# Optimization experiments

Hardware: AMD Instinct MI355X
Metric: run time of the kernel (lower is better)

The kernel has to match this reference:

```python
import jax, jax.numpy as jnp
import numpy as np

B, S, F, D, I, NH, L, K = 8, 512, 64, 512, 1024, 8, 2, 4
DH = I // NH  # 128
H1, OUT = 32, 24


def setup_inputs() -> dict:
    key = jax.random.key(0)
    ks = iter(jax.random.split(key, 48))
    def nrm(shape, s=0.02):
        return jax.random.normal(next(ks), shape, jnp.float32) * s
    return {
        "x": jax.random.normal(next(ks), (B, S, F), jnp.float32),
        "in_w": nrm((F, D)), "in_b": jnp.zeros((D,), jnp.float32),
        "ln_w": jnp.ones((L, D), jnp.float32), "ln_b": jnp.zeros((L, D), jnp.float32),
        "up_w": nrm((L, D, 2 * I)),
        "conv_w": nrm((L, I, K), 0.1), "conv_b": jnp.zeros((L, I), jnp.float32),
        "q_w": nrm((L, I, I)), "k_w": nrm((L, I, I)), "v_w": nrm((L, I, I)),
        "ig_w": nrm((L, 3 * I, NH)), "ig_b": nrm((L, NH), 0.1),
        "fg_w": nrm((L, 3 * I, NH)),
        "fg_b": jnp.tile(jnp.linspace(3.0, 6.0, NH, dtype=jnp.float32)[None], (L, 1)),
        "gn_w": jnp.ones((L, I), jnp.float32),
        "skip_w": jnp.ones((L, I), jnp.float32),
        "down_w": nrm((L, I, D)),
        "post_w": jnp.ones((D,), jnp.float32), "post_b": jnp.zeros((D,), jnp.float32),
        "h1_w": nrm((D, H1)), "h1_b": jnp.zeros((H1,), jnp.float32),
        "h2_w": nrm((H1, OUT)), "h2_b": jnp.zeros((OUT,), jnp.float32),
    }


def _layernorm(x, w, b, eps=1e-5):
    mu = x.mean(-1, keepdims=True)
    var = x.var(-1, keepdims=True)
    return (x - mu) * jax.lax.rsqrt(var + eps) * w + b


def _mlstm(q, k, v, ig, fg):
    # q,k,v: (B,NH,S,DH); ig,fg: (B,NH,S). Parallel exponential-gated matrix memory.
    logf = jax.nn.log_sigmoid(fg)
    cs = jnp.cumsum(logf, axis=-1)                      # (B,NH,S)
    dmat = cs[..., :, None] - cs[..., None, :]          # sum_{j=s+1..t} log f_j
    mask = jnp.tril(jnp.ones((S, S), bool))
    log_fg_mat = jnp.where(mask, dmat, -jnp.inf)
    log_D = log_fg_mat + ig[..., None, :]               # add i-gate at source pos
    max_d = jnp.max(log_D, axis=-1, keepdims=True)      # (B,NH,S,1) stabilizer m
    Dm = jnp.exp(log_D - max_d)
    qk = jnp.einsum('bnsd,bntd->bnst', q, k) / jnp.sqrt(jnp.float32(DH))
    Cmat = qk * Dm
    norm = jnp.maximum(jnp.abs(Cmat.sum(-1, keepdims=True)), jnp.exp(-max_d))
    return jnp.einsum('bnst,bntd->bnsd', Cmat / (norm + 1e-6), v)


def _forward(x, in_w, in_b, ln_w, ln_b, up_w, conv_w, conv_b, q_w, k_w, v_w,
             ig_w, ig_b, fg_w, fg_b, gn_w, skip_w, down_w, post_w, post_b,
             h1_w, h1_b, h2_w, h2_b):
    h = x @ in_w + in_b                                  # input_proj: (B,S,D)
    for l in range(L):                                   # mLSTM block stack
        xn = _layernorm(h, ln_w[l], ln_b[l])
        up = xn @ up_w[l]                                # (B,S,2I)
        x_m, z = up[..., :I], up[..., I:]
        xp = jnp.pad(x_m, ((0, 0), (K - 1, 0), (0, 0)))  # causal depthwise conv1d
        conv = sum(xp[:, j:j + S, :] * conv_w[l][:, j] for j in range(K)) + conv_b[l]
        conv_act = jax.nn.silu(conv)
        q = conv_act @ q_w[l]
        kk = conv_act @ k_w[l]
        v = x_m @ v_w[l]
        qkv = jnp.concatenate([q, kk, v], axis=-1)       # (B,S,3I)
        ig = (qkv @ ig_w[l] + ig_b[l]).transpose(0, 2, 1)  # (B,NH,S)
        fg = (qkv @ fg_w[l] + fg_b[l]).transpose(0, 2, 1)
        to_h = lambda t: t.reshape(B, S, NH, DH).transpose(0, 2, 1, 3)
        hc = _mlstm(to_h(q), to_h(kk), to_h(v), ig, fg)  # (B,NH,S,DH)
        hc = hc.transpose(0, 2, 1, 3)                    # (B,S,NH,DH)
        mu = hc.mean(-1, keepdims=True)                  # per-head layernorm (no bias)
        var = hc.var(-1, keepdims=True)
        hn = ((hc - mu) * jax.lax.rsqrt(var + 1e-5) * gn_w[l].reshape(NH, DH)).reshape(B, S, I)
        hs = (hn + skip_w[l] * conv_act) * jax.nn.silu(z)
        h = h + hs @ down_w[l]                           # residual (dropout=eval identity)
    h = _layernorm(h, post_w, post_b)                    # post-blocks norm
    last = h[:, -1, :]                                   # (B,D)
    return jax.nn.relu(last @ h1_w + h1_b) @ h2_w + h2_b  # output head -> (B,OUT)


def reference(x, in_w, in_b, ln_w, ln_b, up_w, conv_w, conv_b, q_w, k_w, v_w,
              ig_w, ig_b, fg_w, fg_b, gn_w, skip_w, down_w, post_w, post_b,
              h1_w, h1_b, h2_w, h2_b):
    return _forward(x, in_w, in_b, ln_w, ln_b, up_w, conv_w, conv_b, q_w, k_w, v_w,
                    ig_w, ig_b, fg_w, fg_b, gn_w, skip_w, down_w, post_w, post_b,
                    h1_w, h1_b, h2_w, h2_b)
```

## Files before the change

### kernel.cpp

```cpp
#include <hip/hip_runtime.h>
#include <math.h>

#define BB 8
#define SS 512
#define FF 64
#define DD 512
#define II 1024
#define NHH 8
#define KK 4
#define DHH 128
#define H1H 32
#define OUTO 24
#define BS (BB*SS)

typedef unsigned short ushort;
typedef __attribute__((ext_vector_type(8))) short short8;
typedef __attribute__((ext_vector_type(8))) unsigned short ushort8;
typedef __attribute__((ext_vector_type(4))) unsigned short ushort4v;
typedef __attribute__((ext_vector_type(4))) float f32x4;

__device__ __forceinline__ float bf2f(ushort u) {
  return __uint_as_float(((unsigned int)u) << 16);
}
__device__ __forceinline__ ushort f2bf(float f) {
  unsigned int u = __float_as_uint(f);
  unsigned int r = u + 0x7fffu + ((u >> 16) & 1u);
  return (ushort)(r >> 16);
}

typedef __attribute__((address_space(1))) const void gvoid;
typedef __attribute__((address_space(3))) void lvoid;
__device__ __forceinline__ void async16(const void* g, void* l) {
  __builtin_amdgcn_global_load_lds((gvoid*)g, (lvoid*)l, 16, 0, 0);
}

__global__ __launch_bounds__(256) void k_in_proj(const float* __restrict__ x,
                                                 const float* __restrict__ w,
                                                 const float* __restrict__ b,
                                                 float* __restrict__ h) {
  int r0 = blockIdx.x * 16;
  int tid = threadIdx.x;
  __shared__ float xs[16][FF];
  for (int i = tid; i < 16 * FF; i += 256)
    xs[i >> 6][i & 63] = x[(size_t)(r0 + (i >> 6)) * FF + (i & 63)];
  __syncthreads();
  float acc0[16], acc1[16];
  float b0 = b[tid], b1 = b[tid + 256];
#pragma unroll
  for (int r = 0; r < 16; ++r) { acc0[r] = b0; acc1[r] = b1; }
  for (int f = 0; f < FF; ++f) {
    float w0 = w[(size_t)f * DD + tid];
    float w1 = w[(size_t)f * DD + tid + 256];
#pragma unroll
    for (int r = 0; r < 16; ++r) {
      float xv = xs[r][f];
      acc0[r] += xv * w0;
      acc1[r] += xv * w1;
    }
  }
#pragma unroll
  for (int r = 0; r < 16; ++r) {
    h[(size_t)(r0 + r) * DD + tid] = acc0[r];
    h[(size_t)(r0 + r) * DD + tid + 256] = acc1[r];
  }
}

__global__ __launch_bounds__(256) void k_layernorm(const float* __restrict__ in,
                                                   const float* __restrict__ w,
                                                   const float* __restrict__ b,
                                                   ushort* __restrict__ out) {
  int row = blockIdx.x;
  int tid = threadIdx.x;
  float v0 = in[(size_t)row * DD + tid];
  float v1 = in[(size_t)row * DD + tid + 256];
  float s = v0 + v1, sq = v0 * v0 + v1 * v1;
  for (int off = 32; off; off >>= 1) {
    s += __shfl_down(s, off);
    sq += __shfl_down(sq, off);
  }
  __shared__ float ss[4], sqs[4];
  int wid = tid >> 6, lane = tid & 63;
  if (lane == 0) { ss[wid] = s; sqs[wid] = sq; }
  __syncthreads();
  if (tid == 0) {
    ss[0] = ss[0] + ss[1] + ss[2] + ss[3];
    sqs[0] = sqs[0] + sqs[1] + sqs[2] + sqs[3];
  }
  __syncthreads();
  float mean = ss[0] * (1.0f / DD);
  float var = sqs[0] * (1.0f / DD) - mean * mean;
  float r = rsqrtf(var + 1e-5f);
  out[(size_t)row * DD + tid] = f2bf((v0 - mean) * r * w[tid] + b[tid]);
  out[(size_t)row * DD + tid + 256] = f2bf((v1 - mean) * r * w[tid + 256] + b[tid + 256]);
}

__global__ __launch_bounds__(256) void k_wt_all(const float* __restrict__ up_w,
                                                const float* __restrict__ q_w,
                                                const float* __restrict__ k_w,
                                                const float* __restrict__ v_w,
                                                const float* __restrict__ dn_w,
                                                const float* __restrict__ igw,
                                                const float* __restrict__ fgw,
                                                ushort* __restrict__ wt_up,
                                                ushort* __restrict__ wt_qk,
                                                ushort* __restrict__ wt_v,
                                                ushort* __restrict__ wt_dn,
                                                ushort* __restrict__ Wg) {
  int blk = blockIdx.x;
  int l = blk / 4620;
  blk -= l * 4620;
  int tid = threadIdx.x;
  if (blk >= 4608) {
    const float* igwl = igw + (size_t)l * 3 * II * NHH;
    const float* fgwl = fgw + (size_t)l * 3 * II * NHH;
    ushort* Wgl = Wg + (size_t)l * 16 * 3 * II;
    int k = (blk - 4608) * 256 + tid;
    if (k < 3 * II) {
#pragma unroll
      for (int o = 0; o < NHH; ++o) {
        Wgl[(size_t)o * (3 * II) + k] = f2bf(igwl[(size_t)k * NHH + o]);
        Wgl[(size_t)(NHH + o) * (3 * II) + k] = f2bf(fgwl[(size_t)k * NHH + o]);
      }
    }
    return;
  }
  const float* src; ushort* dst; int N, Kd, t;
  if (blk < 1024)      { src = up_w + (size_t)l * DD * 2 * II; dst = wt_up + (size_t)l * 1048576; N = 2048; Kd = 512;  t = blk; }
  else if (blk < 2048) { src = q_w + (size_t)l * II * II;  dst = wt_qk + (size_t)l * 2097152; N = 1024; Kd = 1024; t = blk - 1024; }
  else if (blk < 3072) { src = k_w + (size_t)l * II * II;  dst = wt_qk + (size_t)l * 2097152 + 1024 * 1024; N = 1024; Kd = 1024; t = blk - 2048; }
  else if (blk < 4096) { src = v_w + (size_t)l * II * II;  dst = wt_v + (size_t)l * 1048576;  N = 1024; Kd = 1024; t = blk - 3072; }
  else                 { src = dn_w + (size_t)l * II * DD; dst = wt_dn + (size_t)l * 524288;  N = 512;  Kd = 1024; t = blk - 4096; }
  int ntn = N >> 5;
  int n0 = (t % ntn) * 32, k0 = (t / ntn) * 32;
  __shared__ float tb[32][33];
  int c = tid & 31, r8 = tid >> 5;
  for (int rr = r8; rr < 32; rr += 8)
    tb[rr][c] = src[(size_t)(k0 + rr) * N + n0 + c];
  __syncthreads();
  for (int rr = r8; rr < 32; rr += 8)
    dst[(size_t)(n0 + rr) * Kd + k0 + c] = f2bf(tb[c][rr]);
}

__device__ __forceinline__ void gemm_core8(const ushort* __restrict__ Ag,
                                           const ushort* __restrict__ Bg,
                                           int nkt, ushort* AsB, ushort* BsB,
                                           int woff, int apo, int bpo,
                                           f32x4 (&acc)[2][4]) {
#define STAGE8(p) { int kt_ = (p) * 32; int bi_ = (p) & 3; \
    async16(Ag + kt_, AsB + bi_ * 4096 + woff); \
    async16(Bg + kt_, BsB + bi_ * 4096 + woff); }
  if (0 < nkt) STAGE8(0);
  if (1 < nkt) STAGE8(1);
  if (2 < nkt) STAGE8(2);
  for (int it = 0; it < nkt; ++it) {
    int bey = nkt - 1 - it;
    if (bey >= 2)      asm volatile("s_waitcnt vmcnt(4)" ::: "memory");
    else if (bey == 1) asm volatile("s_waitcnt vmcnt(2)" ::: "memory");
    else               asm volatile("s_waitcnt vmcnt(0)" ::: "memory");
    __builtin_amdgcn_s_barrier();
    int bi = it & 3;
    const ushort* ap = AsB + bi * 4096 + apo;
    const ushort* bp = BsB + bi * 4096 + bpo;
    short8 a[2], b[4];
#pragma unroll
    for (int i = 0; i < 2; ++i) a[i] = *(const short8*)(ap + i * 16 * 32);
#pragma unroll
    for (int j = 0; j < 4; ++j) b[j] = *(const short8*)(bp + j * 16 * 32);
#pragma unroll
    for (int i = 0; i < 2; ++i)
#pragma unroll
      for (int j = 0; j < 4; ++j)
        acc[i][j] = __builtin_amdgcn_mfma_f32_16x16x32_bf16(a[i], b[j], acc[i][j], 0, 0, 0);
    if (it + 3 < nkt) STAGE8(it + 3);
  }
#undef STAGE8
}

__device__ __forceinline__ int swz_scol(int lane) {
  return (((lane & 3) ^ ((lane >> 3) & 3)) * 8);
}
__device__ __forceinline__ int swz_fk(int lane) {
  return ((((lane >> 4) ^ (lane >> 1)) & 3) * 8);
}
__device__ __forceinline__ void xcd_swz(int* bx, int* by) {
  int gx = gridDim.x;
  int nwg = gx * gridDim.y;
  int orig = blockIdx.y * gx + blockIdx.x;
  int q = nwg >> 3;
  int wgid = (orig & 7) * q + (orig >> 3);
  *bx = wgid % gx;
  *by = wgid / gx;
}

__global__ __launch_bounds__(512) void k_gemm_up(const ushort* __restrict__ A,
                                                 const ushort* __restrict__ Bt,
                                                 ushort* __restrict__ Cb) {
  __shared__ ushort As[4][4096];
  __shared__ ushort Bs[4][4096];
  int tid = threadIdx.x;
  int wave = tid >> 6, lane = tid & 63;
  int wm = wave >> 1, wn = wave & 1;
  int bx, by; xcd_swz(&bx, &by);
  int m0 = by * 128, n0 = bx * 128;
  int srow = wave * 16 + (lane >> 2), scol = swz_scol(lane);
  const ushort* Ag = A + (size_t)(m0 + srow) * DD + scol;
  const ushort* Bg = Bt + (size_t)(n0 + srow) * DD + scol;
  int woff = wave * 512;
  int frow = lane & 15, fk = swz_fk(lane);
  int apo = (wm * 32 + frow) * 32 + fk;
  int bpo = (wn * 64 + frow) * 32 + fk;
  f32x4 acc[2][4] = {};
  gemm_core8(Ag, Bg, DD / 32, &As[0][0], &Bs[0][0], woff, apo, bpo, acc);
  int ccol = lane & 15, crow = (lane >> 4) * 4;
#pragma unroll
  for (int i = 0; i < 2; ++i)
#pragma unroll
    for (int j = 0; j < 4; ++j) {
      int grow = m0 + wm * 32 + i * 16 + crow;
      int gcol = n0 + wn * 64 + j * 16 + ccol;
#pragma unroll
      for (int r = 0; r < 4; ++r)
        Cb[(size_t)(grow + r) * 2048 + gcol] = f2bf(acc[i][j][r]);
    }
}

__global__ __launch_bounds__(512) void k_gemm_qkv(const ushort* __restrict__ convb,
                                                  const ushort* __restrict__ upb,
                                                  const ushort* __restrict__ wt_qk,
                                                  const ushort* __restrict__ wt_v,
                                                  ushort* __restrict__ qkb,
                                                  ushort* __restrict__ vb,
                                                  ushort* __restrict__ vbt) {
  __shared__ ushort As[4][4096];
  __shared__ ushort Bs[4][4096];
  int tid = threadIdx.x;
  int wave = tid >> 6, lane = tid & 63;
  int wm = wave >> 1, wn = wave & 1;
  int bx, by; xcd_swz(&bx, &by);
  int isv = bx >= 16;
  int m0 = by * 128;
  int n0 = (isv ? bx - 16 : bx) * 128;
  const ushort* A = isv ? upb : convb;
  int lda = isv ? 2048 : 1024;
  const ushort* Bt = isv ? wt_v : wt_qk;
  int srow = wave * 16 + (lane >> 2), scol = swz_scol(lane);
  const ushort* Ag = A + (size_t)(m0 + srow) * lda + scol;
  const ushort* Bg = Bt + (size_t)(n0 + srow) * II + scol;
  int woff = wave * 512;
  int frow = lane & 15, fk = swz_fk(lane);
  int apo = (wm * 32 + frow) * 32 + fk;
  int bpo = (wn * 64 + frow) * 32 + fk;
  f32x4 acc[2][4] = {};
  gemm_core8(Ag, Bg, II / 32, &As[0][0], &Bs[0][0], woff, apo, bpo, acc);
  int ccol = lane & 15, crow = (lane >> 4) * 4;
#pragma unroll
  for (int i = 0; i < 2; ++i)
#pragma unroll
    for (int j = 0; j < 4; ++j) {
      int grow = m0 + wm * 32 + i * 16 + crow;
      int gcol = n0 + wn * 64 + j * 16 + ccol;
      if (!isv) {
#pragma unroll
        for (int r = 0; r < 4; ++r)
          qkb[(size_t)(grow + r) * 2048 + gcol] = f2bf(acc[i][j][r]);
      } else {
#pragma unroll
        for (int r = 0; r < 4; ++r)
          vb[(size_t)(grow + r) * II + gcol] = f2bf(acc[i][j][r]);
        int b8 = grow >> 9, sloc = grow & 511;
        int nh = gcol >> 7, d = gcol & 127;
        ushort4v o;
#pragma unroll
        for (int r = 0; r < 4; ++r) o[r] = f2bf(acc[i][j][r]);
        *(ushort4v*)&vbt[((size_t)(b8 * NHH + nh) * DHH + d) * SS + sloc] = o;
      }
    }
}

__global__ __launch_bounds__(512) void k_gemm_down(const ushort* __restrict__ A,
                                                   const ushort* __restrict__ Bt,
                                                   float* __restrict__ Cf) {
  __shared__ ushort As[4][4096];
  __shared__ ushort Bs[4][4096];
  int tid = threadIdx.x;
  int wave = tid >> 6, lane = tid & 63;
  int wm = wave >> 1, wn = wave & 1;
  int bx, by; xcd_swz(&bx, &by);
  int m0 = by * 128, n0 = bx * 128;
  int k0 = blockIdx.z * 256;
  int srow = wave * 16 + (lane >> 2), scol = swz_scol(lane);
  const ushort* Ag = A + (size_t)(m0 + srow) * II + k0 + scol;
  const ushort* Bg = Bt + (size_t)(n0 + srow) * II + k0 + scol;
  int woff = wave * 512;
  int frow = lane & 15, fk = swz_fk(lane);
  int apo = (wm * 32 + frow) * 32 + fk;
  int bpo = (wn * 64 + frow) * 32 + fk;
  f32x4 acc[2][4] = {};
  gemm_core8(Ag, Bg, 256 / 32, &As[0][0], &Bs[0][0], woff, apo, bpo, acc);
  int ccol = lane & 15, crow = (lane >> 4) * 4;
#pragma unroll
  for (int i = 0; i < 2; ++i)
#pragma unroll
    for (int j = 0; j < 4; ++j) {
      int grow = m0 + wm * 32 + i * 16 + crow;
      int gcol = n0 + wn * 64 + j * 16 + ccol;
#pragma unroll
      for (int r = 0; r < 4; ++r)
        atomicAdd(&Cf[(size_t)(grow + r) * DD + gcol], acc[i][j][r]);
    }
}

__global__ __launch_bounds__(256) void k_conv_silu(const ushort* __restrict__ up,
                                                   const float* __restrict__ cw,
                                                   const float* __restrict__ cb,
                                                   ushort* __restrict__ out) {
  int g = blockIdx.x * 256 + threadIdx.x;
  int c8 = (g & 127) * 8;
  int row = g >> 7;
  int s = row & (SS - 1);
  float acc[8];
  float4 wv[8];
#pragma unroll
  for (int t = 0; t < 8; ++t) {
    acc[t] = cb[c8 + t];
    wv[t] = *(const float4*)(cw + (size_t)(c8 + t) * 4);
  }
#pragma unroll
  for (int j = 0; j < 4; ++j) {
    int so = s + j - 3;
    if (so >= 0) {
      ushort8 u = *(const ushort8*)&up[(size_t)(row + j - 3) * 2048 + c8];
#pragma unroll
      for (int t = 0; t < 8; ++t) {
        float wc = (j == 0) ? wv[t].x : (j == 1) ? wv[t].y : (j == 2) ? wv[t].z : wv[t].w;
        acc[t] += bf2f(u[t]) * wc;
      }
    }
  }
  ushort8 o;
#pragma unroll
  for (int t = 0; t < 8; ++t) {
    float sig = 1.0f / (1.0f + __expf(-acc[t]));
    o[t] = f2bf(acc[t] * sig);
  }
  *(ushort8*)&out[(size_t)row * II + c8] = o;
}

__global__ __launch_bounds__(64) void k_gates_mfma(const ushort* __restrict__ qkb,
                                                   const ushort* __restrict__ vb,
                                                   const ushort* __restrict__ Wg,
                                                   const float* __restrict__ igb,
                                                   const float* __restrict__ fgb,
                                                   float* __restrict__ ig,
                                                   float* __restrict__ fg) {
  int lane = threadIdx.x;
  int row0 = blockIdx.x * 16;
  int l15 = lane & 15, lg = lane >> 4;
  int arow = row0 + l15;
  const ushort* qrow = qkb + (size_t)arow * 2048 + lg * 8;
  const ushort* vrow = vb + (size_t)arow * II + lg * 8;
  const ushort* wrow = Wg + (size_t)l15 * (3 * II) + lg * 8;
  f32x4 acc0 = {}, acc1 = {};
#pragma unroll 4
  for (int k = 0; k < 2048; k += 64) {
    short8 a0 = *(const short8*)(qrow + k);
    short8 b0 = *(const short8*)(wrow + k);
    short8 a1 = *(const short8*)(qrow + k + 32);
    short8 b1 = *(const short8*)(wrow + k + 32);
    acc0 = __builtin_amdgcn_mfma_f32_16x16x32_bf16(a0, b0, acc0, 0, 0, 0);
    acc1 = __builtin_amdgcn_mfma_f32_16x16x32_bf16(a1, b1, acc1, 0, 0, 0);
  }
#pragma unroll 4
  for (int k = 0; k < 1024; k += 64) {
    short8 a0 = *(const short8*)(vrow + k);
    short8 b0 = *(const short8*)(wrow + 2048 + k);
    short8 a1 = *(const short8*)(vrow + k + 32);
    short8 b1 = *(const short8*)(wrow + 2048 + k + 32);
    acc0 = __builtin_amdgcn_mfma_f32_16x16x32_bf16(a0, b0, acc0, 0, 0, 0);
    acc1 = __builtin_amdgcn_mfma_f32_16x16x32_bf16(a1, b1, acc1, 0, 0, 0);
  }
  int o = l15;
#pragma unroll
  for (int r = 0; r < 4; ++r) {
    int row = row0 + lg * 4 + r;
    int bb = row >> 9, s = row & (SS - 1);
    float val = acc0[r] + acc1[r];
    if (o < NHH)
      ig[((size_t)bb * NHH + o) * SS + s] = val + igb[o];
    else
      fg[((size_t)bb * NHH + (o - NHH)) * SS + s] = val + fgb[o - NHH];
  }
}

__global__ __launch_bounds__(64) void k_scan(const float* __restrict__ ig,
                                             const float* __restrict__ fg,
                                             float* __restrict__ e_g, float* __restrict__ M_g,
                                             float* __restrict__ maxd_g) {
  int bn = blockIdx.x;
  int lane = threadIdx.x;
  size_t base = (size_t)bn * SS + lane * 8;
  float4 f0 = *(const float4*)&fg[base];
  float4 f1 = *(const float4*)&fg[base + 4];
  float fv[8] = {f0.x, f0.y, f0.z, f0.w, f1.x, f1.y, f1.z, f1.w};
  float lf[8];
#pragma unroll
  for (int j = 0; j < 8; ++j) {
    float f = fv[j];
    lf[j] = (f >= 0.f) ? -log1pf(expf(-f)) : (f - log1pf(expf(f)));
  }
  float cum[8];
  float run = 0.f;
#pragma unroll
  for (int j = 0; j < 8; ++j) { run += lf[j]; cum[j] = run; }
  float inc = run;
#pragma unroll
  for (int off = 1; off < 64; off <<= 1) {
    float t = __shfl_up(inc, off);
    if (lane >= off) inc += t;
  }
  float exs = inc - run;
  float4 i0 = *(const float4*)&ig[base];
  float4 i1 = *(const float4*)&ig[base + 4];
  float igv[8] = {i0.x, i0.y, i0.z, i0.w, i1.x, i1.y, i1.z, i1.w};
  float cs[8], e[8];
#pragma unroll
  for (int j = 0; j < 8; ++j) {
    cs[j] = exs + cum[j];
    e[j] = igv[j] - cs[j];
  }
  float mcum[8];
  float mrun = -3.0e38f;
#pragma unroll
  for (int j = 0; j < 8; ++j) { mrun = fmaxf(mrun, e[j]); mcum[j] = mrun; }
  float minc = mrun;
#pragma unroll
  for (int off = 1; off < 64; off <<= 1) {
    float t = __shfl_up(minc, off);
    if (lane >= off) minc = fmaxf(minc, t);
  }
  float mex = __shfl_up(minc, 1);
  if (lane == 0) mex = -3.0e38f;
  float M[8], mdv[8];
#pragma unroll
  for (int j = 0; j < 8; ++j) {
    M[j] = fmaxf(mex, mcum[j]);
    mdv[j] = cs[j] + M[j];
  }
  *(float4*)&e_g[base] = make_float4(e[0], e[1], e[2], e[3]);
  *(float4*)&e_g[base + 4] = make_float4(e[4], e[5], e[6], e[7]);
  *(float4*)&M_g[base] = make_float4(M[0], M[1], M[2], M[3]);
  *(float4*)&M_g[base + 4] = make_float4(M[4], M[5], M[6], M[7]);
  *(float4*)&maxd_g[base] = make_float4(mdv[0], mdv[1], mdv[2], mdv[3]);
  *(float4*)&maxd_g[base + 4] = make_float4(mdv[4], mdv[5], mdv[6], mdv[7]);
}

__global__ __launch_bounds__(256) void k_attn_mfma(const ushort* __restrict__ qkb,
                                                   const ushort* __restrict__ vbt,
                                                   const float* __restrict__ e_g,
                                                   const float* __restrict__ M_g,
                                                   const float* __restrict__ maxd_g,
                                                   const ushort* __restrict__ convact,
                                                   const ushort* __restrict__ up,
                                                   const float* __restrict__ gnw,
                                                   const float* __restrict__ skw,
                                                   ushort* __restrict__ hs) {
  __shared__ __align__(16) ushort K2[2][64 * 128];
  __shared__ __align__(16) ushort V2[2][128 * 64];
  __shared__ __align__(16) ushort w_s[4][16 * 72];
  __shared__ float e_s[SS];

  int tid = threadIdx.x;
  int wave = tid >> 6, lane = tid & 63;
  int xb = blockIdx.x;
  int stile = (xb & 1) ? (7 - (xb >> 1)) : (xb >> 1);
  int bn = blockIdx.y;
  int b = bn >> 3, n = bn & 7;
  int s0 = stile * 64;

  const size_t qbase = (size_t)(b * SS) * 2048 + (size_t)n * DHH;
  const size_t kbase = qbase + II;
  const size_t vtbase = (size_t)bn * DHH * SS;

  int l15 = lane & 15, lg = lane >> 4;
  int kg8 = lg * 8;
  int crow = lg * 4;
  int srow_base = s0 + wave * 16 + crow;

  e_s[tid] = e_g[(size_t)bn * SS + tid];
  e_s[tid + 256] = e_g[(size_t)bn * SS + tid + 256];

  short8 qf[4];
  {
    int qrow = s0 + wave * 16 + l15;
#pragma unroll
    for (int ks = 0; ks < 4; ++ks)
      qf[ks] = *(const short8*)&qkb[qbase + (size_t)qrow * 2048 + ks * 32 + kg8];
  }
  float Ms[4], md[4];
#pragma unroll
  for (int r = 0; r < 4; ++r) {
    Ms[r] = M_g[(size_t)bn * SS + srow_base + r];
    md[r] = maxd_g[(size_t)bn * SS + srow_base + r];
  }

  f32x4 acc[8] = {};
  float rsum[4] = {};
  const float rsq = 0.08838834764831845f;
  ushort* w_w = &w_s[wave][0];
  int ntt = stile + 1;

#pragma unroll
  for (int i = 0; i < 4; ++i) {
    int r = wave * 16 + i * 4 + (lane >> 4);
    int sp = (lane & 15) ^ (r & 7);
    async16(&qkb[kbase + (size_t)r * 2048 + sp * 8], &K2[0][(wave * 16 + i * 4) * 128]);
  }
#pragma unroll
  for (int i = 0; i < 4; ++i) {
    int d = wave * 32 + i * 8 + (lane >> 3);
    int sp = (lane & 7) ^ (d & 7);
    async16(&vbt[vtbase + (size_t)d * SS + sp * 8], &V2[0][(wave * 32 + i * 8) * 64]);
  }

  for (int tt = 0; tt < ntt; ++tt) {
    int cur = tt & 1;
    if (tt + 1 < ntt) {
      int t1 = (tt + 1) * 64;
      int nxt = cur ^ 1;
#pragma unroll
      for (int i = 0; i < 4; ++i) {
        int r = wave * 16 + i * 4 + (lane >> 4);
        int sp = (lane & 15) ^ (r & 7);
        async16(&qkb[kbase + (size_t)(t1 + r) * 2048 + sp * 8], &K2[nxt][(wave * 16 + i * 4) * 128]);
      }
#pragma unroll
      for (int i = 0; i < 4; ++i) {
        int d = wave * 32 + i * 8 + (lane >> 3);
        int sp = (lane & 7) ^ (d & 7);
        async16(&vbt[vtbase + (size_t)d * SS + t1 + sp * 8], &V2[nxt][(wave * 32 + i * 8) * 64]);
      }
      asm volatile("s_waitcnt vmcnt(8) lgkmcnt(0)" ::: "memory");
    } else {
      asm volatile("s_waitcnt vmcnt(0) lgkmcnt(0)" ::: "memory");
    }
    __builtin_amdgcn_s_barrier();

    int t0 = tt * 64;
    const ushort* Kc = &K2[cur][0];
    const ushort* Vc = &V2[cur][0];

    f32x4 s4[4];
#pragma unroll
    for (int ct = 0; ct < 4; ++ct) {
      f32x4 c = {};
      int ro = l15 + 16 * ct;
#pragma unroll
      for (int ks = 0; ks < 4; ++ks) {
        int sp = (ks * 4 + lg) ^ (ro & 7);
        short8 kf = *(const short8*)&Kc[ro * 128 + sp * 8];
        c = __builtin_amdgcn_mfma_f32_16x16x32_bf16(qf[ks], kf, c, 0, 0, 0);
      }
      s4[ct] = c;
    }
#pragma unroll
    for (int ct = 0; ct < 4; ++ct) {
      int t = t0 + l15 + 16 * ct;
      float e = e_s[t];
#pragma unroll
      for (int r = 0; r < 4; ++r) {
        int s = srow_base + r;
        float val = (t <= s) ? s4[ct][r] * rsq * __expf(e - Ms[r]) : 0.f;
        s4[ct][r] = val;
        w_w[(crow + r) * 72 + l15 + 16 * ct] = f2bf(val);
      }
    }
#pragma unroll
    for (int r = 0; r < 4; ++r) {
      float tmp = s4[0][r] + s4[1][r] + s4[2][r] + s4[3][r];
      tmp += __shfl_xor(tmp, 1);
      tmp += __shfl_xor(tmp, 2);
      tmp += __shfl_xor(tmp, 4);
      tmp += __shfl_xor(tmp, 8);
      rsum[r] += tmp;
    }
    short8 wf0 = *(const short8*)&w_w[l15 * 72 + kg8];
    short8 wf1 = *(const short8*)&w_w[l15 * 72 + 32 + kg8];
#pragma unroll
    for (int dt = 0; dt < 8; ++dt) {
      int d = dt * 16 + l15;
      int sp0 = lg ^ (d & 7);
      int sp1 = (lg + 4) ^ (d & 7);
      short8 vf0 = *(const short8*)&Vc[d * 64 + sp0 * 8];
      short8 vf1 = *(const short8*)&Vc[d * 64 + sp1 * 8];
      acc[dt] = __builtin_amdgcn_mfma_f32_16x16x32_bf16(wf0, vf0, acc[dt], 0, 0, 0);
      acc[dt] = __builtin_amdgcn_mfma_f32_16x16x32_bf16(wf1, vf1, acc[dt], 0, 0, 0);
    }
    __builtin_amdgcn_s_barrier();
  }

  float scl[4], sum[4] = {}, sq[4] = {};
#pragma unroll
  for (int r = 0; r < 4; ++r) {
    float nrm = fmaxf(fabsf(rsum[r]), __expf(-md[r]));
    scl[r] = 1.0f / (nrm + 1e-6f);
  }
#pragma unroll
  for (int dt = 0; dt < 8; ++dt)
#pragma unroll
    for (int r = 0; r < 4; ++r) {
      float v = acc[dt][r] * scl[r];
      sum[r] += v;
      sq[r] += v * v;
    }
#pragma unroll
  for (int r = 0; r < 4; ++r) {
#pragma unroll
    for (int off = 1; off <= 8; off <<= 1) {
      sum[r] += __shfl_xor(sum[r], off);
      sq[r] += __shfl_xor(sq[r], off);
    }
  }
  float mu[4], rstd[4];
#pragma unroll
  for (int r = 0; r < 4; ++r) {
    mu[r] = sum[r] * (1.0f / DHH);
    float var = sq[r] * (1.0f / DHH) - mu[r] * mu[r];
    rstd[r] = rsqrtf(var + 1e-5f);
  }
#pragma unroll
  for (int dt = 0; dt < 8; ++dt) {
    int c = dt * 16 + l15;
    float gw = gnw[n * DHH + c];
    float sw = skw[n * DHH + c];
#pragma unroll
    for (int r = 0; r < 4; ++r) {
      size_t ridx = (size_t)(b * SS + srow_base + r);
      float v = acc[dt][r] * scl[r];
      float hn = (v - mu[r]) * rstd[r] * gw;
      float ca = bf2f(convact[ridx * II + n * DHH + c]);
      float z = bf2f(up[ridx * 2048 + II + n * DHH + c]);
      float sz = z / (1.0f + __expf(-z));
      hs[ridx * II + n * DHH + c] = f2bf((hn + sw * ca) * sz);
    }
  }
}

__global__ __launch_bounds__(256) void k_head(const float* __restrict__ h,
                                              const float* __restrict__ pw,
                                              const float* __restrict__ pb,
                                              const float* __restrict__ w1,
                                              const float* __restrict__ b1,
                                              const float* __restrict__ w2,
                                              const float* __restrict__ b2,
                                              float* __restrict__ out) {
  int b = blockIdx.x;
  int tid = threadIdx.x;
  __shared__ float last[DD];
  __shared__ float hid[H1H];
  __shared__ float ss[4], sqs[4];
  const float* row = h + ((size_t)b * SS + SS - 1) * DD;
  float v0 = row[tid], v1 = row[tid + 256];
  float s = v0 + v1, sq = v0 * v0 + v1 * v1;
  for (int off = 32; off; off >>= 1) {
    s += __shfl_down(s, off);
    sq += __shfl_down(sq, off);
  }
  int wid = tid >> 6, lane = tid & 63;
  if (lane == 0) { ss[wid] = s; sqs[wid] = sq; }
  __syncthreads();
  if (tid == 0) {
    ss[0] = ss[0] + ss[1] + ss[2] + ss[3];
    sqs[0] = sqs[0] + sqs[1] + sqs[2] + sqs[3];
  }
  __syncthreads();
  float mean = ss[0] * (1.0f / DD);
  float var = sqs[0] * (1.0f / DD) - mean * mean;
  float r = rsqrtf(var + 1e-5f);
  last[tid] = (v0 - mean) * r * pw[tid] + pb[tid];
  last[tid + 256] = (v1 - mean) * r * pw[tid + 256] + pb[tid + 256];
  __syncthreads();
  if (tid < H1H) {
    float a = b1[tid];
    for (int d2 = 0; d2 < DD; ++d2) a += last[d2] * w1[(size_t)d2 * H1H + tid];
    hid[tid] = fmaxf(a, 0.f);
  }
  __syncthreads();
  if (tid < OUTO) {
    float a = b2[tid];
#pragma unroll
    for (int j2 = 0; j2 < H1H; ++j2) a += hid[j2] * w2[(size_t)j2 * OUTO + tid];
    out[(size_t)b * OUTO + tid] = a;
  }
}

extern "C" void kernel_launch(void* const* d_in, const int* in_sizes, int n_in,
                              void* d_out, int out_size, void* d_ws, size_t ws_size,
                              hipStream_t stream) {
  (void)in_sizes; (void)n_in; (void)out_size; (void)ws_size;
  const float* x    = (const float*)d_in[0];
  const float* in_w = (const float*)d_in[1];
  const float* in_b = (const float*)d_in[2];
  const float* ln_w = (const float*)d_in[3];
  const float* ln_b = (const float*)d_in[4];
  const float* up_w = (const float*)d_in[5];
  const float* conv_w = (const float*)d_in[6];
  const float* conv_b = (const float*)d_in[7];
  const float* q_w  = (const float*)d_in[8];
  const float* k_w  = (const float*)d_in[9];
  const float* v_w  = (const float*)d_in[10];
  const float* ig_w = (const float*)d_in[11];
  const float* ig_b = (const float*)d_in[12];
  const float* fg_w = (const float*)d_in[13];
  const float* fg_b = (const float*)d_in[14];
  const float* gn_w = (const float*)d_in[15];
  const float* sk_w = (const float*)d_in[16];
  const float* dn_w = (const float*)d_in[17];
  const float* po_w = (const float*)d_in[18];
  const float* po_b = (const float*)d_in[19];
  const float* h1_w = (const float*)d_in[20];
  const float* h1_b = (const float*)d_in[21];
  const float* h2_w = (const float*)d_in[22];
  const float* h2_b = (const float*)d_in[23];

  float* h = (float*)d_ws;
  ushort* xn_bf = (ushort*)(h + 2097152);
  ushort* up_bf = xn_bf + 2097152;
  ushort* conv_bf = up_bf + 8388608;
  ushort* qkb = conv_bf + 4194304;
  ushort* vb = qkb + 8388608;
  ushort* vbt = vb + 4194304;
  ushort* hs_bf = vbt + 4194304;
  ushort* wt_up = hs_bf + 4194304;
  ushort* wt_qk = wt_up + 2097152;
  ushort* wt_v  = wt_qk + 4194304;
  ushort* wt_dn = wt_v + 2097152;
  ushort* Wg = wt_dn + 1048576;
  float* igb_ = (float*)(Wg + 98304);
  float* fgb_ = igb_ + 32768;
  float* e_g  = fgb_ + 32768;
  float* M_g  = e_g + 32768;
  float* md_g = M_g + 32768;

  k_in_proj<<<BS / 16, 256, 0, stream>>>(x, in_w, in_b, h);
  k_wt_all<<<9240, 256, 0, stream>>>(up_w, q_w, k_w, v_w, dn_w, ig_w, fg_w,
                                     wt_up, wt_qk, wt_v, wt_dn, Wg);
  for (int l = 0; l < 2; ++l) {
    k_layernorm<<<BS, 256, 0, stream>>>(h, ln_w + l * DD, ln_b + l * DD, xn_bf);
    k_gemm_up<<<dim3(16, 32), 512, 0, stream>>>(xn_bf, wt_up + (size_t)l * 1048576, up_bf);
    k_conv_silu<<<BS * II / 8 / 256, 256, 0, stream>>>(up_bf, conv_w + l * II * KK,
                                                       conv_b + l * II, conv_bf);
    k_gemm_qkv<<<dim3(24, 32), 512, 0, stream>>>(conv_bf, up_bf,
                                                 wt_qk + (size_t)l * 2097152,
                                                 wt_v + (size_t)l * 1048576,
                                                 qkb, vb, vbt);
    k_gates_mfma<<<256, 64, 0, stream>>>(qkb, vb, Wg + (size_t)l * 49152,
                                         ig_b + l * NHH, fg_b + l * NHH, igb_, fgb_);
    k_scan<<<BB * NHH, 64, 0, stream>>>(igb_, fgb_, e_g, M_g, md_g);
    k_attn_mfma<<<dim3(8, BB * NHH), 256, 0, stream>>>(qkb, vbt, e_g, M_g, md_g,
                                                       conv_bf, up_bf,
                                                       gn_w + l * II, sk_w + l * II, hs_bf);
    k_gemm_down<<<dim3(4, 32, 4), 512, 0, stream>>>(hs_bf, wt_dn + (size_t)l * 524288, h);
  }
  k_head<<<BB, 256, 0, stream>>>(h, po_w, po_b, h1_w, h1_b, h2_w, h2_b, (float*)d_out);
}
```

Before: 378.2 us.

## Enlarge QKV GEMM tile to 256x128 with 3-stage inline async pipeline

The QKV projection GEMM now computes 256x128 output tiles per block instead of 128x128, with each wave owning a 64x64 sub-tile (4x4 MFMA accumulators). The grid is halved along M to match. The shared gemm_core8 call is replaced by an inlined 3-stage async copy pipeline using explicit vmcnt waits. The aim is more reuse of each loaded B tile and a deeper prefetch. In exchange, register pressure and LDS use per block go up, and with fewer blocks (384) the GPU may be less well occupied.

```diff
diff --git a/kernel.cpp b/kernel.cpp
--- a/kernel.cpp
+++ b/kernel.cpp
@@ -231,33 +231,61 @@
                                                   ushort* __restrict__ qkb,
                                                   ushort* __restrict__ vb,
                                                   ushort* __restrict__ vbt) {
-  __shared__ ushort As[4][4096];
-  __shared__ ushort Bs[4][4096];
+  __shared__ ushort As[3][8192];
+  __shared__ ushort Bs[3][4096];
   int tid = threadIdx.x;
   int wave = tid >> 6, lane = tid & 63;
   int wm = wave >> 1, wn = wave & 1;
   int bx, by; xcd_swz(&bx, &by);
   int isv = bx >= 16;
-  int m0 = by * 128;
+  int m0 = by * 256;
   int n0 = (isv ? bx - 16 : bx) * 128;
   const ushort* A = isv ? upb : convb;
   int lda = isv ? 2048 : 1024;
   const ushort* Bt = isv ? wt_v : wt_qk;
-  int srow = wave * 16 + (lane >> 2), scol = swz_scol(lane);
-  const ushort* Ag = A + (size_t)(m0 + srow) * lda + scol;
-  const ushort* Bg = Bt + (size_t)(n0 + srow) * II + scol;
-  int woff = wave * 512;
+  int scol = swz_scol(lane);
+  const ushort* Ag1 = A + (size_t)(m0 + wave * 32 + (lane >> 2)) * lda + scol;
+  const ushort* Ag2 = Ag1 + (size_t)16 * lda;
+  const ushort* Bg = Bt + (size_t)(n0 + wave * 16 + (lane >> 2)) * II + scol;
+  ushort* AsB = &As[0][0];
+  ushort* BsB = &Bs[0][0];
   int frow = lane & 15, fk = swz_fk(lane);
-  int apo = (wm * 32 + frow) * 32 + fk;
+  int apo = (wm * 64 + frow) * 32 + fk;
   int bpo = (wn * 64 + frow) * 32 + fk;
-  f32x4 acc[2][4] = {};
-  gemm_core8(Ag, Bg, II / 32, &As[0][0], &Bs[0][0], woff, apo, bpo, acc);
+  f32x4 acc[4][4] = {};
+  const int nkt = II / 32;
+#define STAGEQ(p) { int kt_ = (p) * 32; int bi_ = (p) % 3; \
+    async16(Ag1 + kt_, AsB + bi_ * 8192 + wave * 1024); \
+    async16(Ag2 + kt_, AsB + bi_ * 8192 + wave * 1024 + 512); \
+    async16(Bg + kt_, BsB + bi_ * 4096 + wave * 512); }
+  STAGEQ(0);
+  STAGEQ(1);
+  for (int it = 0; it < nkt; ++it) {
+    if (it < nkt - 1) asm volatile("s_waitcnt vmcnt(3)" ::: "memory");
+    else              asm volatile("s_waitcnt vmcnt(0)" ::: "memory");
+    __builtin_amdgcn_s_barrier();
+    if (it + 2 < nkt) STAGEQ(it + 2);
+    int bi = it % 3;
+    const ushort* ap = AsB + bi * 8192 + apo;
+    const ushort* bp = BsB + bi * 4096 + bpo;
+    short8 a[4], b[4];
+#pragma unroll
+    for (int i = 0; i < 4; ++i) a[i] = *(const short8*)(ap + i * 16 * 32);
+#pragma unroll
+    for (int j = 0; j < 4; ++j) b[j] = *(const short8*)(bp + j * 16 * 32);
+#pragma unroll
+    for (int i = 0; i < 4; ++i)
+#pragma unroll
+      for (int j = 0; j < 4; ++j)
+        acc[i][j] = __builtin_amdgcn_mfma_f32_16x16x32_bf16(a[i], b[j], acc[i][j], 0, 0, 0);
+  }
+#undef STAGEQ
   int ccol = lane & 15, crow = (lane >> 4) * 4;
 #pragma unroll
-  for (int i = 0; i < 2; ++i)
+  for (int i = 0; i < 4; ++i)
 #pragma unroll
     for (int j = 0; j < 4; ++j) {
-      int grow = m0 + wm * 32 + i * 16 + crow;
+      int grow = m0 + wm * 64 + i * 16 + crow;
       int gcol = n0 + wn * 64 + j * 16 + ccol;
       if (!isv) {
 #pragma unroll
@@ -749,7 +777,7 @@
     k_gemm_up<<<dim3(16, 32), 512, 0, stream>>>(xn_bf, wt_up + (size_t)l * 1048576, up_bf);
     k_conv_silu<<<BS * II / 8 / 256, 256, 0, stream>>>(up_bf, conv_w + l * II * KK,
                                                        conv_b + l * II, conv_bf);
-    k_gemm_qkv<<<dim3(24, 32), 512, 0, stream>>>(conv_bf, up_bf,
+    k_gemm_qkv<<<dim3(24, 16), 512, 0, stream>>>(conv_bf, up_bf,
                                                  wt_qk + (size_t)l * 2097152,
                                                  wt_v + (size_t)l * 1048576,
                                                  qkb, vb, vbt);
```

New measurement: 408.8 us. 1.08x slower.
